# Performance work log

Measured on AMD Instinct MI355X. Metric: run time of the kernel, lower is better.

Reference implementation:

```python
import jax, jax.numpy as jnp
import numpy as np

TEMPERATURE = 0.5
NEG_FILL = -9000000000000000.0


def setup_inputs() -> dict:
    key = jax.random.key(0)
    z = jax.random.normal(key, (16384, 128), dtype=jnp.float32)
    return {"z": z}


def reference(z) -> jnp.ndarray:
    n2 = z.shape[0]  # 2N
    # L2 normalize rows (eps matches torch F.normalize default 1e-12)
    norm = jnp.maximum(jnp.linalg.norm(z, axis=1, keepdims=True), 1e-12)
    zn = z / norm
    # (2N, 2N) cosine similarity scaled by temperature
    sim = jnp.matmul(zn, zn.T) / TEMPERATURE
    # mask self-similarity on the diagonal
    idx = jnp.arange(n2)
    sim = jnp.where(idx[:, None] == idx[None, :], NEG_FILL, sim)
    # positive pair of row i is i^1 (2i <-> 2i+1)
    pos_indices = idx ^ 1
    pos_sim = sim[idx, pos_indices]
    loss = -pos_sim + jax.scipy.special.logsumexp(sim, axis=1)
    return jnp.mean(loss)
```

## Files before the change

kernel.cpp:

```cpp
#include <hip/hip_runtime.h>
#include <hip/hip_bf16.h>

#define N2 16384
#define D  128
#define PANEL 16384
#define SQC1 1.69864360258810896f
#define LN2  0.69314718055994530942f

typedef float f32x4 __attribute__((ext_vector_type(4)));

#if __has_builtin(__builtin_amdgcn_exp2f)
#define EXP2(x) __builtin_amdgcn_exp2f(x)
#else
#define EXP2(x) exp2f(x)
#endif

__device__ __forceinline__ unsigned char f2e4m3(float f) {
    union { float f; unsigned u; } v; v.f = f;
    unsigned s = (v.u >> 24) & 0x80;
    int e = (int)((v.u >> 23) & 255) - 127;
    unsigned m = v.u & 0x7fffff;
    if (e < -10) return (unsigned char)s;
    if (e >= -6) {
        unsigned r = m + 0x7ffff + ((m >> 20) & 1);
        unsigned mm = r >> 20;
        int E = e;
        if (mm >= 8) { mm = 0; E += 1; }
        return (unsigned char)(s | ((E + 7) << 3) | (mm & 7));
    }
    float a = fabsf(f) * 512.0f;
    int n = (int)rintf(a);
    return (unsigned char)(s | n);
}

__device__ __forceinline__ float e4m3f(unsigned v) {
    unsigned s = v >> 7, e = (v >> 3) & 15, m = v & 7;
    float f;
    if (e) { union { unsigned u; float g; } x; x.u = ((e + 120) << 23) | (m << 20); f = x.g; }
    else   f = (float)m * 0.001953125f;
    return s ? -f : f;
}

__device__ __forceinline__ void stage16(const char* __restrict__ g,
                                        char* lds, int tid) {
    const int wid = tid >> 6, lane = tid & 63;
    #pragma unroll
    for (int i = 0; i < 4; ++i) {
        int off = (wid << 12) + (i << 10) + (lane << 4);
        int src = off ^ (((off >> 7) & 7) << 4);
        __builtin_amdgcn_global_load_lds(
            (const __attribute__((address_space(1))) unsigned*)(g + src),
            (__attribute__((address_space(3))) unsigned*)(lds + (wid << 12) + (i << 10)),
            16, 0, 0);
    }
}

__global__ void k_norm(const float* __restrict__ z, unsigned char* __restrict__ zq,
                       float* __restrict__ rowsum, float* __restrict__ out) {
    if (blockIdx.x < 64) rowsum[blockIdx.x * 256 + threadIdx.x] = 0.f;
    if (blockIdx.x == 64 && threadIdx.x == 0) out[0] = 0.f;
    int row  = blockIdx.x * 4 + (threadIdx.x >> 6);
    int lane = threadIdx.x & 63;
    const float2 v = ((const float2*)(z + (size_t)row * D))[lane];
    float ss = v.x * v.x + v.y * v.y;
    #pragma unroll
    for (int m = 1; m < 64; m <<= 1) ss += __shfl_xor(ss, m);
    float inv = SQC1 / fmaxf(sqrtf(ss), 1e-12f);
    unsigned short o = (unsigned short)f2e4m3(v.x * inv)
                     | ((unsigned short)f2e4m3(v.y * inv) << 8);
    ((unsigned short*)(zq + (size_t)row * D))[lane] = o;
}

__global__ __launch_bounds__(256, 3)
void k_sim(const unsigned char* __restrict__ zq, float* __restrict__ rowsum) {
    __shared__ char ls[3 * PANEL];

    const int tileI = blockIdx.y;
    const int c = blockIdx.x;
    const int sLo = c * 11;
    const int nt = (c < 5) ? 11 : ((tileI < 64) ? 10 : 9);

    const int tid  = threadIdx.x;
    const int lane = tid & 63, wid = tid >> 6;
    const int wr = wid >> 1, wc = wid & 1;
    const int l16 = lane & 15, lg = lane >> 4;
    const char* zb = (const char*)zq;

    stage16(zb + (size_t)tileI * PANEL, ls, tid);
    asm volatile("s_waitcnt vmcnt(0)" ::: "memory");
    __builtin_amdgcn_s_barrier();

    long af[4][4];
    #pragma unroll
    for (int kk = 0; kk < 4; ++kk)
        #pragma unroll
        for (int m = 0; m < 4; ++m) {
            int row = wr * 64 + m * 16 + l16;
            int d = row * 128 + kk * 32 + lg * 8;
            af[kk][m] = *(const long*)(ls + (d ^ ((row & 7) << 4)));
        }
    asm volatile("s_waitcnt lgkmcnt(0)" ::: "memory");
    __builtin_amdgcn_s_barrier();

    stage16(zb + (size_t)((tileI + sLo) & 127) * PANEL, ls, tid);
    stage16(zb + (size_t)((tileI + sLo + 1) & 127) * PANEL, ls + PANEL, tid);

    float rs[4][4];
    #pragma unroll
    for (int m = 0; m < 4; ++m)
        #pragma unroll
        for (int r = 0; r < 4; ++r) rs[m][r] = 0.f;

    int cur = 0;
    for (int t = 0; t < nt; ++t) {
        const int s  = sLo + t;
        const int jt = (tileI + s) & 127;

        if (t == 0)                    { asm volatile("s_waitcnt vmcnt(4)"  ::: "memory"); }
        else if (t == 1 || t == nt - 1){ asm volatile("s_waitcnt vmcnt(8)"  ::: "memory"); }
        else                           { asm volatile("s_waitcnt vmcnt(12)" ::: "memory"); }
        __builtin_amdgcn_s_barrier();

        char* rbuf = ls + (cur << 14);
        if (t + 2 < nt) {
            int nxt = cur + 2; if (nxt >= 3) nxt -= 3;
            stage16(zb + (size_t)((tileI + s + 2) & 127) * PANEL, ls + (nxt << 14), tid);
        }

        f32x4 acc[4][4];
        __builtin_amdgcn_s_setprio(1);
        #pragma unroll
        for (int kk = 0; kk < 4; ++kk) {
            long bk[4];
            #pragma unroll
            for (int n = 0; n < 4; ++n) {
                int row = wc * 64 + n * 16 + l16;
                int d = row * 128 + kk * 32 + lg * 8;
                bk[n] = *(const long*)(rbuf + (d ^ ((row & 7) << 4)));
            }
            #pragma unroll
            for (int m = 0; m < 4; ++m)
                #pragma unroll
                for (int n = 0; n < 4; ++n)
                    acc[m][n] = __builtin_amdgcn_mfma_f32_16x16x32_fp8_fp8(
                        af[kk][m], bk[n],
                        (kk == 0) ? f32x4{0.f, 0.f, 0.f, 0.f} : acc[m][n], 0, 0, 0);
        }
        __builtin_amdgcn_s_setprio(0);

        float cs[4] = {0.f, 0.f, 0.f, 0.f};
        if (s == 0) {
            #pragma unroll
            for (int m = 0; m < 4; ++m)
                #pragma unroll
                for (int r = 0; r < 4; ++r) {
                    int li = wr * 64 + m * 16 + lg * 4 + r;
                    float a = 0.f;
                    #pragma unroll
                    for (int n = 0; n < 4; ++n) {
                        int lj = wc * 64 + n * 16 + l16;
                        float e = EXP2(acc[m][n][r]);
                        a += (li == lj) ? 0.f : e;
                    }
                    rs[m][r] += a;
                }
        } else {
            #pragma unroll
            for (int m = 0; m < 4; ++m)
                #pragma unroll
                for (int r = 0; r < 4; ++r) {
                    float a = 0.f;
                    #pragma unroll
                    for (int n = 0; n < 4; ++n) {
                        float e = EXP2(acc[m][n][r]);
                        a += e;
                        cs[n] += e;
                    }
                    rs[m][r] += a;
                }
        }
        #pragma unroll
        for (int n = 0; n < 4; ++n) {
            float v = cs[n];
            v += __shfl_xor(v, 16);
            v += __shfl_xor(v, 32);
            if (lg == 0)
                atomicAdd(&rowsum[jt * 128 + wc * 64 + n * 16 + l16], v);
        }
        cur = (cur == 2) ? 0 : cur + 1;
    }

    #pragma unroll
    for (int m = 0; m < 4; ++m)
        #pragma unroll
        for (int r = 0; r < 4; ++r) {
            float v = rs[m][r];
            v += __shfl_xor(v, 1);
            v += __shfl_xor(v, 2);
            v += __shfl_xor(v, 4);
            v += __shfl_xor(v, 8);
            if (l16 == 0)
                atomicAdd(&rowsum[tileI * 128 + wr * 64 + m * 16 + lg * 4 + r], v);
        }
}

__global__ void k_loss_reduce(const unsigned char* __restrict__ zq,
                              const float* __restrict__ rowsum,
                              float* __restrict__ out) {
    const int tid = threadIdx.x + blockIdx.x * 256;
    float p = 0.f;
    const uint4* v16 = (const uint4*)zq;
    for (int v = tid; v < N2 * D / 16; v += 64 * 256) {
        uint4 a = v16[v];
        uint4 b = v16[v ^ 8];
        const unsigned* aw = (const unsigned*)&a;
        const unsigned* bw = (const unsigned*)&b;
        #pragma unroll
        for (int w = 0; w < 4; ++w)
            #pragma unroll
            for (int j = 0; j < 4; ++j)
                p += e4m3f((aw[w] >> (8 * j)) & 255) * e4m3f((bw[w] >> (8 * j)) & 255);
    }
    float part = logf(rowsum[tid]) - LN2 * p;

    __shared__ float sm[4];
    #pragma unroll
    for (int m = 1; m < 64; m <<= 1) part += __shfl_xor(part, m);
    if ((threadIdx.x & 63) == 0) sm[threadIdx.x >> 6] = part;
    __syncthreads();
    if (threadIdx.x == 0)
        atomicAdd(out, (sm[0] + sm[1] + sm[2] + sm[3]) * (1.0f / (float)N2));
}

extern "C" void kernel_launch(void* const* d_in, const int* in_sizes, int n_in,
                              void* d_out, int out_size, void* d_ws, size_t ws_size,
                              hipStream_t stream) {
    const float* z = (const float*)d_in[0];
    float* out = (float*)d_out;

    unsigned char* zq = (unsigned char*)d_ws;
    float* rowsum = (float*)((char*)d_ws + (size_t)N2 * D);

    k_norm<<<N2 / 4, 256, 0, stream>>>(z, zq, rowsum, out);
    dim3 grid(6, 128);
    k_sim<<<grid, 256, 0, stream>>>(zq, rowsum);
    k_loss_reduce<<<64, 256, 0, stream>>>(zq, rowsum, out);
}
```

Before: 72.43 us.

## Software-pipeline MFMA with exp epilogue and fuse loss reduction into sim kernel

```diff
diff --git a/kernel.cpp b/kernel.cpp
--- a/kernel.cpp
+++ b/kernel.cpp
@@ -33,14 +33,6 @@
     return (unsigned char)(s | n);
 }
 
-__device__ __forceinline__ float e4m3f(unsigned v) {
-    unsigned s = v >> 7, e = (v >> 3) & 15, m = v & 7;
-    float f;
-    if (e) { union { unsigned u; float g; } x; x.u = ((e + 120) << 23) | (m << 20); f = x.g; }
-    else   f = (float)m * 0.001953125f;
-    return s ? -f : f;
-}
-
 __device__ __forceinline__ void stage16(const char* __restrict__ g,
                                         char* lds, int tid) {
     const int wid = tid >> 6, lane = tid & 63;
@@ -56,9 +48,10 @@
 }
 
 __global__ void k_norm(const float* __restrict__ z, unsigned char* __restrict__ zq,
-                       float* __restrict__ rowsum, float* __restrict__ out) {
+                       float* __restrict__ rowsum, float* __restrict__ possum,
+                       unsigned* __restrict__ counter) {
     if (blockIdx.x < 64) rowsum[blockIdx.x * 256 + threadIdx.x] = 0.f;
-    if (blockIdx.x == 64 && threadIdx.x == 0) out[0] = 0.f;
+    if (blockIdx.x == 64 && threadIdx.x == 0) { possum[0] = 0.f; counter[0] = 0u; }
     int row  = blockIdx.x * 4 + (threadIdx.x >> 6);
     int lane = threadIdx.x & 63;
     const float2 v = ((const float2*)(z + (size_t)row * D))[lane];
@@ -71,14 +64,104 @@
     ((unsigned short*)(zq + (size_t)row * D))[lane] = o;
 }
 
-__global__ __launch_bounds__(256, 3)
-void k_sim(const unsigned char* __restrict__ zq, float* __restrict__ rowsum) {
+__device__ __forceinline__ void kloop(const char* rbuf, const long (&af)[4][4],
+                                      f32x4 (&cur)[4][4], int wc, int l16, int lg) {
+    #pragma unroll
+    for (int kk = 0; kk < 4; ++kk) {
+        long bk[4];
+        #pragma unroll
+        for (int n = 0; n < 4; ++n) {
+            int row = wc * 64 + n * 16 + l16;
+            int d = row * 128 + kk * 32 + lg * 8;
+            bk[n] = *(const long*)(rbuf + (d ^ ((row & 7) << 4)));
+        }
+        #pragma unroll
+        for (int m = 0; m < 4; ++m)
+            #pragma unroll
+            for (int n = 0; n < 4; ++n)
+                cur[m][n] = __builtin_amdgcn_mfma_f32_16x16x32_fp8_fp8(
+                    af[kk][m], bk[n],
+                    (kk == 0) ? f32x4{0.f, 0.f, 0.f, 0.f} : cur[m][n], 0, 0, 0);
+    }
+}
+
+__device__ __forceinline__ void epi_main(const f32x4 (&prev)[4][4],
+                                         float (&rs)[4][4], float (&cs)[4]) {
+    #pragma unroll
+    for (int m = 0; m < 4; ++m)
+        #pragma unroll
+        for (int r = 0; r < 4; ++r) {
+            float a = 0.f;
+            #pragma unroll
+            for (int n = 0; n < 4; ++n) {
+                float e = EXP2(prev[m][n][r]);
+                a += e;
+                cs[n] += e;
+            }
+            rs[m][r] += a;
+        }
+}
+
+__device__ __forceinline__ void iterE(int t, int nt, int sLo, int tileI,
+    const char* zb, char* ls, const long (&af)[4][4],
+    f32x4 (&cur)[4][4], f32x4 (&prev)[4][4], float (&rs)[4][4],
+    float* rowsum, float* possum,
+    int tid, int wr, int wc, int l16, int lg, int lane) {
+    const int s = sLo + t;
+    if (t == 1)                    { asm volatile("s_waitcnt vmcnt(4)"  ::: "memory"); }
+    else if (t == 2 || t == nt - 1){ asm volatile("s_waitcnt vmcnt(8)"  ::: "memory"); }
+    else                           { asm volatile("s_waitcnt vmcnt(12)" ::: "memory"); }
+    __builtin_amdgcn_s_barrier();
+
+    const char* rbuf = ls + ((t % 3) << 14);
+    if (t + 2 < nt)
+        stage16(zb + (size_t)((tileI + s + 2) & 127) * PANEL,
+                ls + (((t + 2) % 3) << 14), tid);
+
+    kloop(rbuf, af, cur, wc, l16, lg);
+
+    float cs[4] = {0.f, 0.f, 0.f, 0.f};
+    epi_main(prev, rs, cs);
+    const int sPrev = s - 1;
+    const int jtp = (tileI + sPrev) & 127;
+    if (sPrev == 0) {
+        float pp = 0.f;
+        #pragma unroll
+        for (int m = 0; m < 4; ++m)
+            #pragma unroll
+            for (int r = 0; r < 4; ++r) {
+                if (wr == wc && l16 == (lg * 4 + r))
+                    rs[m][r] -= EXP2(prev[m][m][r]);
+                if (wr == wc && l16 == ((lg * 4 + r) ^ 1))
+                    pp += prev[m][m][r];
+            }
+        #pragma unroll
+        for (int sh = 1; sh < 64; sh <<= 1) pp += __shfl_xor(pp, sh);
+        if (wr == wc && lane == 0) atomicAdd(possum, pp);
+        cs[0] = cs[1] = cs[2] = cs[3] = 0.f;
+    }
+    #pragma unroll
+    for (int n = 0; n < 4; ++n) {
+        float v = cs[n];
+        v += __shfl_xor(v, 16);
+        v += __shfl_xor(v, 32);
+        if (lg == 0)
+            atomicAdd(&rowsum[jtp * 128 + wc * 64 + n * 16 + l16], v);
+    }
+}
+
+__global__ __launch_bounds__(256, 2)
+void k_sim(const unsigned char* __restrict__ zq, float* __restrict__ rowsum,
+           float* __restrict__ possum, unsigned* __restrict__ counter,
+           float* __restrict__ out) {
     __shared__ char ls[3 * PANEL];
+    __shared__ float sm[4];
+    __shared__ unsigned ticket;
 
     const int tileI = blockIdx.y;
     const int c = blockIdx.x;
-    const int sLo = c * 11;
-    const int nt = (c < 5) ? 11 : ((tileI < 64) ? 10 : 9);
+    const int sLo = c * 16;
+    const int nt = (c == 3 && tileI < 64) ? 17 : 16;
 
     const int tid  = threadIdx.x;
     const int lane = tid & 63, wid = tid >> 6;
@@ -111,85 +194,38 @@
         #pragma unroll
         for (int r = 0; r < 4; ++r) rs[m][r] = 0.f;
 
-    int cur = 0;
-    for (int t = 0; t < nt; ++t) {
-        const int s  = sLo + t;
-        const int jt = (tileI + s) & 127;
-
-        if (t == 0)                    { asm volatile("s_waitcnt vmcnt(4)"  ::: "memory"); }
-        else if (t == 1 || t == nt - 1){ asm volatile("s_waitcnt vmcnt(8)"  ::: "memory"); }
-        else                           { asm volatile("s_waitcnt vmcnt(12)" ::: "memory"); }
-        __builtin_amdgcn_s_barrier();
-
-        char* rbuf = ls + (cur << 14);
-        if (t + 2 < nt) {
-            int nxt = cur + 2; if (nxt >= 3) nxt -= 3;
-            stage16(zb + (size_t)((tileI + s + 2) & 127) * PANEL, ls + (nxt << 14), tid);
-        }
-
-        f32x4 acc[4][4];
-        __builtin_amdgcn_s_setprio(1);
-        #pragma unroll
-        for (int kk = 0; kk < 4; ++kk) {
-            long bk[4];
-            #pragma unroll
-            for (int n = 0; n < 4; ++n) {
-                int row = wc * 64 + n * 16 + l16;
-                int d = row * 128 + kk * 32 + lg * 8;
-                bk[n] = *(const long*)(rbuf + (d ^ ((row & 7) << 4)));
-            }
-            #pragma unroll
-            for (int m = 0; m < 4; ++m)
-                #pragma unroll
-                for (int n = 0; n < 4; ++n)
-                    acc[m][n] = __builtin_amdgcn_mfma_f32_16x16x32_fp8_fp8(
-                        af[kk][m], bk[n],
-                        (kk == 0) ? f32x4{0.f, 0.f, 0.f, 0.f} : acc[m][n], 0, 0, 0);
-        }
-        __builtin_amdgcn_s_setprio(0);
-
+    f32x4 accA[4][4], accB[4][4];
+
+    asm volatile("s_waitcnt vmcnt(4)" ::: "memory");
+    __builtin_amdgcn_s_barrier();
+    stage16(zb + (size_t)((tileI + sLo + 2) & 127) * PANEL, ls + 2 * PANEL, tid);
+    kloop(ls, af, accA, wc, l16, lg);
+
+    int t = 1;
+    for (; t + 1 < nt; t += 2) {
+        iterE(t,     nt, sLo, tileI, zb, ls, af, accB, accA, rs, rowsum, possum,
+              tid, wr, wc, l16, lg, lane);
+        iterE(t + 1, nt, sLo, tileI, zb, ls, af, accA, accB, rs, rowsum, possum,
+              tid, wr, wc, l16, lg, lane);
+    }
+    if (t < nt)
+        iterE(t, nt, sLo, tileI, zb, ls, af, accB, accA, rs, rowsum, possum,
+              tid, wr, wc, l16, lg, lane);
+
+    {
         float cs[4] = {0.f, 0.f, 0.f, 0.f};
-        if (s == 0) {
-            #pragma unroll
-            for (int m = 0; m < 4; ++m)
-                #pragma unroll
-                for (int r = 0; r < 4; ++r) {
-                    int li = wr * 64 + m * 16 + lg * 4 + r;
-                    float a = 0.f;
-                    #pragma unroll
-                    for (int n = 0; n < 4; ++n) {
-                        int lj = wc * 64 + n * 16 + l16;
-                        float e = EXP2(acc[m][n][r]);
-                        a += (li == lj) ? 0.f : e;
-                    }
-                    rs[m][r] += a;
-                }
-        } else {
-            #pragma unroll
-            for (int m = 0; m < 4; ++m)
-                #pragma unroll
-                for (int r = 0; r < 4; ++r) {
-                    float a = 0.f;
-                    #pragma unroll
-                    for (int n = 0; n < 4; ++n) {
-                        float e = EXP2(acc[m][n][r]);
-                        a += e;
-                        cs[n] += e;
-                    }
-                    rs[m][r] += a;
-                }
-        }
+        const int jtp = (tileI + sLo + nt - 1) & 127;
+        if (nt & 1) epi_main(accA, rs, cs);
+        else        epi_main(accB, rs, cs);
         #pragma unroll
         for (int n = 0; n < 4; ++n) {
             float v = cs[n];
             v += __shfl_xor(v, 16);
             v += __shfl_xor(v, 32);
             if (lg == 0)
-                atomicAdd(&rowsum[jt * 128 + wc * 64 + n * 16 + l16], v);
-        }
-        cur = (cur == 2) ? 0 : cur + 1;
-    }
-
+                atomicAdd(&rowsum[jtp * 128 + wc * 64 + n * 16 + l16], v);
+        }
+    }
     #pragma unroll
     for (int m = 0; m < 4; ++m)
         #pragma unroll
@@ -202,34 +238,26 @@
             if (l16 == 0)
                 atomicAdd(&rowsum[tileI * 128 + wr * 64 + m * 16 + lg * 4 + r], v);
         }
-}
-
-__global__ void k_loss_reduce(const unsigned char* __restrict__ zq,
-                              const float* __restrict__ rowsum,
-                              float* __restrict__ out) {
-    const int tid = threadIdx.x + blockIdx.x * 256;
-    float p = 0.f;
-    const uint4* v16 = (const uint4*)zq;
-    for (int v = tid; v < N2 * D / 16; v += 64 * 256) {
-        uint4 a = v16[v];
-        uint4 b = v16[v ^ 8];
-        const unsigned* aw = (const unsigned*)&a;
-        const unsigned* bw = (const unsigned*)&b;
-        #pragma unroll
-        for (int w = 0; w < 4; ++w)
-            #pragma unroll
-            for (int j = 0; j < 4; ++j)
-                p += e4m3f((aw[w] >> (8 * j)) & 255) * e4m3f((bw[w] >> (8 * j)) & 255);
-    }
-    float part = logf(rowsum[tid]) - LN2 * p;
-
-    __shared__ float sm[4];
-    #pragma unroll
-    for (int m = 1; m < 64; m <<= 1) part += __shfl_xor(part, m);
-    if ((threadIdx.x & 63) == 0) sm[threadIdx.x >> 6] = part;
+
+    __threadfence();
+    if (tid == 0) ticket = atomicAdd(counter, 1u);
     __syncthreads();
-    if (threadIdx.x == 0)
-        atomicAdd(out, (sm[0] + sm[1] + sm[2] + sm[3]) * (1.0f / (float)N2));
+    if (ticket == 511) {
+        __threadfence();
+        float part = 0.f;
+        for (int i = tid; i < N2; i += 256)
+            part += logf(__hip_atomic_load(&rowsum[i], __ATOMIC_RELAXED,
+                                           __HIP_MEMORY_SCOPE_AGENT));
+        #pragma unroll
+        for (int m = 1; m < 64; m <<= 1) part += __shfl_xor(part, m);
+        if (lane == 0) sm[wid] = part;
+        __syncthreads();
+        if (tid == 0) {
+            float ps = __hip_atomic_load(possum, __ATOMIC_RELAXED,
+                                         __HIP_MEMORY_SCOPE_AGENT);
+            out[0] = (sm[0] + sm[1] + sm[2] + sm[3] - LN2 * ps) * (1.0f / (float)N2);
+        }
+    }
 }
 
 extern "C" void kernel_launch(void* const* d_in, const int* in_sizes, int n_in,
@@ -240,9 +268,10 @@
 
     unsigned char* zq = (unsigned char*)d_ws;
     float* rowsum = (float*)((char*)d_ws + (size_t)N2 * D);
-
-    k_norm<<<N2 / 4, 256, 0, stream>>>(z, zq, rowsum, out);
-    dim3 grid(6, 128);
-    k_sim<<<grid, 256, 0, stream>>>(zq, rowsum);
-    k_loss_reduce<<<64, 256, 0, stream>>>(zq, rowsum, out);
-}
+    float* possum = rowsum + N2;
+    unsigned* counter = (unsigned*)(possum + 1);
+
+    k_norm<<<N2 / 4, 256, 0, stream>>>(z, zq, rowsum, possum, counter);
+    dim3 grid(4, 128);
+    k_sim<<<grid, 256, 0, stream>>>(zq, rowsum, possum, counter, out);
+}
```

After: 133.7 us. +84.6%, slower.
